# Kernel tuning notes

Hardware: AMD Instinct MI355X
Metric: run time of the kernel (lower is better)

## Reference

```python
import jax, jax.numpy as jnp
import numpy as np

N_NODES = 100000


def setup_inputs() -> dict:
    key = jax.random.key(0)
    ks = jax.random.split(key, 6)
    F_IN, F_CH, F_OUT = 64, 64, 64
    E = 1200000
    x = jax.random.normal(ks[0], (N_NODES, F_IN), dtype=jnp.float32)
    edge_index = jax.random.randint(ks[1], (2, E), 0, N_NODES, dtype=jnp.int64)
    # MLP params (PyTorch Linear default init scale ~ 1/sqrt(fan_in))
    s1 = 1.0 / np.sqrt(2 * F_IN)
    s2 = 1.0 / np.sqrt(F_CH)
    W1 = jax.random.uniform(ks[2], (2 * F_IN, F_CH), jnp.float32, -s1, s1)
    b1 = jax.random.uniform(ks[3], (F_CH,), jnp.float32, -s1, s1)
    W2 = jax.random.uniform(ks[4], (F_CH, F_OUT), jnp.float32, -s2, s2)
    b2 = jax.random.uniform(ks[5], (F_OUT,), jnp.float32, -s2, s2)
    return {"x": x, "edge_index": edge_index, "W1": W1, "b1": b1, "W2": W2, "b2": b2}


def reference(x, edge_index, W1, b1, W2, b2):
    # PyG EdgeConv with aggr='add': out_i = sum_j MLP(concat[x_i, x_j - x_i])
    src = edge_index[0]  # j (source / neighbor)
    dst = edge_index[1]  # i (target, aggregation index)
    x_i = x[dst]                     # [E, F]
    x_j = x[src]                     # [E, F]
    msg = jnp.concatenate([x_i, x_j - x_i], axis=-1)      # [E, 2F]
    h = jax.nn.relu(msg @ W1 + b1) @ W2 + b2               # [E, F_out]
    agg = jax.ops.segment_sum(h, dst, num_segments=N_NODES)  # [N, F_out]
    return jnp.tanh(agg)
```

## Files before the change

kernel.cpp:

```cpp
#include <hip/hip_runtime.h>
#include <math.h>


#define FDIM 64
#define BN 64
#define BSH 6
#define CAPB 1024
#define MAXB 2048
#define EPB 4096
#define PRE_SMEM 24576

typedef unsigned int u32;
typedef unsigned short u16;
typedef _Float16 hf;
typedef _Float16 h2 __attribute__((ext_vector_type(2)));

__device__ __forceinline__ u32 f2h(float f) {
    union { u16 s; hf h; } c; c.h = (hf)f; return (u32)c.s;
}
__device__ __forceinline__ h2 u2h2(u32 u) {
    union { u32 u; h2 h; } c; c.u = u; return c.h;
}

__global__ __launch_bounds__(256) void prep_k(
    const float* __restrict__ x, const float* __restrict__ W1,
    const float* __restrict__ b1, u16* __restrict__ Ah,
    u16* __restrict__ Bmh, const int* __restrict__ ei,
    u32* __restrict__ slotB, int* __restrict__ gcnt,
    int N, int E, int NB, int nPre, int nBin)
{
    __shared__ __align__(16) char smem[PRE_SMEM];
    const int idx = blockIdx.x;
    const int tid = threadIdx.x;

    if ((idx % 6) == 5) {
        const int bb = idx / 6;
        if (bb >= nBin) return;
        int* histL = (int*)smem;
        int* gbase = histL + MAXB;
        const int e0 = bb * EPB;

        for (int j = tid; j < NB; j += 256) histL[j] = 0;
        __syncthreads();

        #pragma unroll 8
        for (int i = 0; i < EPB / 256; ++i) {
            int e = e0 + i * 256 + tid;
            if (e < E) {
                int d = ei[E + e];
                atomicAdd(&histL[d >> BSH], 1);
            }
        }
        __syncthreads();

        for (int j = tid; j < NB; j += 256) {
            int h = histL[j];
            gbase[j] = (h > 0) ? atomicAdd(&gcnt[j], h) : 0;
            histL[j] = 0;
        }
        __syncthreads();

        #pragma unroll 8
        for (int i = 0; i < EPB / 256; ++i) {
            int e = e0 + i * 256 + tid;
            if (e < E) {
                int s = ei[e];
                int d = ei[E + e];
                int b = d >> BSH;
                int pos = gbase[b] + atomicAdd(&histL[b], 1);
                if (pos < CAPB)
                    slotB[(size_t)b * CAPB + pos] =
                        ((u32)(d & (BN - 1)) << 20) | (u32)s;
            }
        }
        return;
    }

    const int pb = idx - idx / 6;
    if (pb >= nPre) return;
    u32 (*Wch)[128] = (u32(*)[128])smem;
    u32* xs = (u32*)(smem + 16384);

    const int node0 = pb * 64;

    for (int i = tid; i < 4096; i += 256) {
        int kk = i >> 7, c = i & 127;
        int k0 = 2 * kk, k1 = k0 + 1;
        float a0, a1;
        if (c < 64) {
            a0 = W1[k0 * 64 + c] - W1[(64 + k0) * 64 + c];
            a1 = W1[k1 * 64 + c] - W1[(64 + k1) * 64 + c];
        } else {
            int cc = c - 64;
            a0 = W1[(64 + k0) * 64 + cc];
            a1 = W1[(64 + k1) * 64 + cc];
        }
        Wch[kk][c] = f2h(a0) | (f2h(a1) << 16);
    }
    {
        const float4* X4 = (const float4*)x;
        #pragma unroll
        for (int it = 0; it < 4; ++it) {
            int i = it * 256 + tid;
            int n = i >> 4, k4 = i & 15;
            int gn = node0 + n;
            float4 v = make_float4(0.f, 0.f, 0.f, 0.f);
            if (gn < N) v = X4[(size_t)gn * 16 + k4];
            int r0 = 2 * k4, r1 = r0 + 1;
            int g = n >> 2, lo = n & 3;
            xs[r0 * 64 + (((g ^ (r0 & 15)) << 2) | lo)] = f2h(v.x) | (f2h(v.y) << 16);
            xs[r1 * 64 + (((g ^ (r1 & 15)) << 2) | lo)] = f2h(v.z) | (f2h(v.w) << 16);
        }
    }
    __syncthreads();

    const int ng = tid & 15, cg = tid >> 4;
    const int n0 = ng * 4, c0 = cg * 8;

    float acc[4][8];
    #pragma unroll
    for (int ci = 0; ci < 8; ++ci) {
        float init = (c0 < 64) ? b1[c0 + ci] : 0.f;
        #pragma unroll
        for (int ni = 0; ni < 4; ++ni) acc[ni][ci] = init;
    }

    #pragma unroll 4
    for (int kk = 0; kk < 32; ++kk) {
        uint4 xq = *(const uint4*)&xs[kk * 64 + ((ng ^ (kk & 15)) << 2)];
        uint4 w0 = *(const uint4*)&Wch[kk][c0];
        uint4 w1 = *(const uint4*)&Wch[kk][c0 + 4];
        h2 wv[8] = {u2h2(w0.x), u2h2(w0.y), u2h2(w0.z), u2h2(w0.w),
                    u2h2(w1.x), u2h2(w1.y), u2h2(w1.z), u2h2(w1.w)};
        u32 xq4[4] = {xq.x, xq.y, xq.z, xq.w};
        #pragma unroll
        for (int ni = 0; ni < 4; ++ni) {
            h2 xh = u2h2(xq4[ni]);
            #pragma unroll
            for (int ci = 0; ci < 8; ++ci)
                acc[ni][ci] = __builtin_amdgcn_fdot2(xh, wv[ci], acc[ni][ci], false);
        }
    }

    #pragma unroll
    for (int ni = 0; ni < 4; ++ni) {
        int n = node0 + n0 + ni;
        if (n >= N) break;
        uint4 pk;
        pk.x = f2h(acc[ni][0]) | (f2h(acc[ni][1]) << 16);
        pk.y = f2h(acc[ni][2]) | (f2h(acc[ni][3]) << 16);
        pk.z = f2h(acc[ni][4]) | (f2h(acc[ni][5]) << 16);
        pk.w = f2h(acc[ni][6]) | (f2h(acc[ni][7]) << 16);
        if (c0 < 64) *(uint4*)&Ah[(size_t)n * 64 + c0] = pk;
        else         *(uint4*)&Bmh[(size_t)n * 64 + (c0 - 64)] = pk;
    }
}

__global__ __launch_bounds__(256) void fused_agg(
    const u16* __restrict__ Ah, const u16* __restrict__ Bmh,
    const u32* __restrict__ slotB, const int* __restrict__ gcnt,
    const float* __restrict__ W2, const float* __restrict__ b2,
    float* __restrict__ out, int N)
{
    __shared__ __align__(16) char uni[16896];
    __shared__ int histL[BN];
    __shared__ int rowO[BN + 1];
    __shared__ int ofs[BN];
    __shared__ float b2s[64];

    uint2* aggTb = (uint2*)uni;
    u32* csrS = (u32*)(uni + 8704);
    u32* eStage = (u32*)(uni + 12800);
    u32* W2kp = (u32*)(uni + 8704);

    const int tid = threadIdx.x;
    const int b = blockIdx.x;
    const int node0 = b * BN;
    const int cntB = min(gcnt[b], CAPB);

    if (tid < 64) b2s[tid] = b2[tid];
    if (tid < BN) histL[tid] = 0;
    __syncthreads();

    for (int i = tid; i < cntB; i += 256) {
        u32 e = slotB[(size_t)b * CAPB + i];
        eStage[i] = e;
        atomicAdd(&histL[e >> 20], 1);
    }
    __syncthreads();

    if (tid < 32) {
        int l = tid;
        int h0 = histL[2 * l], h1 = histL[2 * l + 1];
        int s = h0 + h1, inc = s;
        #pragma unroll
        for (int off = 1; off < 32; off <<= 1) {
            int t = __shfl_up(inc, off);
            if (l >= off) inc += t;
        }
        int base = inc - s;
        rowO[2 * l] = base; rowO[2 * l + 1] = base + h0;
        ofs[2 * l] = base;  ofs[2 * l + 1] = base + h0;
        if (l == 31) rowO[BN] = inc;
    }
    __syncthreads();

    for (int i = tid; i < cntB; i += 256) {
        u32 e = eStage[i];
        int pos = atomicAdd(&ofs[e >> 20], 1);
        csrS[pos] = e & 0xFFFFFu;
    }
    __syncthreads();

    const int q = tid & 15, ng = tid >> 4;
    {
        const uint2* __restrict__ B2 = (const uint2*)Bmh;
        const uint2* __restrict__ A2 = (const uint2*)Ah;
        const h2 SEL10 = {(_Float16)1.f, (_Float16)0.f};
        const h2 SEL01 = {(_Float16)0.f, (_Float16)1.f};
        const h2 HZ = {(_Float16)0.f, (_Float16)0.f};
        #pragma unroll
        for (int h = 0; h < 4; ++h) {
            int nl = ng * 4 + h;
            int gn = node0 + nl;
            int start = rowO[nl];
            int d = (gn < N) ? (rowO[nl + 1] - start) : 0;
            uint2 ua = make_uint2(0u, 0u);
            if (gn < N) ua = A2[(size_t)gn * 16 + q];
            h2 A0 = u2h2(ua.x), A1 = u2h2(ua.y);
            float ac0 = 0.f, ac1 = 0.f, ac2 = 0.f, ac3 = 0.f;

            int j = 0;
            for (; j + 8 <= d; j += 8) {
                int ss[8];
                uint2 bb[8];
                #pragma unroll
                for (int t = 0; t < 8; ++t) ss[t] = csrS[start + j + t];
                #pragma unroll
                for (int t = 0; t < 8; ++t) bb[t] = B2[(size_t)ss[t] * 16 + q];
                #pragma unroll
                for (int t = 0; t < 8; ++t) {
                    h2 t0 = A0 + u2h2(bb[t].x);
                    h2 t1 = A1 + u2h2(bb[t].y);
                    t0 = __builtin_elementwise_max(t0, HZ);
                    t1 = __builtin_elementwise_max(t1, HZ);
                    ac0 = __builtin_amdgcn_fdot2(t0, SEL10, ac0, false);
                    ac1 = __builtin_amdgcn_fdot2(t0, SEL01, ac1, false);
                    ac2 = __builtin_amdgcn_fdot2(t1, SEL10, ac2, false);
                    ac3 = __builtin_amdgcn_fdot2(t1, SEL01, ac3, false);
                }
            }
            if (j < d) {
                int ss[8];
                uint2 bb[8];
                #pragma unroll
                for (int t = 0; t < 8; ++t) ss[t] = csrS[start + min(j + t, d - 1)];
                #pragma unroll
                for (int t = 0; t < 8; ++t) bb[t] = B2[(size_t)ss[t] * 16 + q];
                #pragma unroll
                for (int t = 0; t < 8; ++t) {
                    if (j + t >= d) { bb[t].x = 0xFC00FC00u; bb[t].y = 0xFC00FC00u; }
                    h2 t0 = A0 + u2h2(bb[t].x);
                    h2 t1 = A1 + u2h2(bb[t].y);
                    t0 = __builtin_elementwise_max(t0, HZ);
                    t1 = __builtin_elementwise_max(t1, HZ);
                    ac0 = __builtin_amdgcn_fdot2(t0, SEL10, ac0, false);
                    ac1 = __builtin_amdgcn_fdot2(t0, SEL01, ac1, false);
                    ac2 = __builtin_amdgcn_fdot2(t1, SEL10, ac2, false);
                    ac3 = __builtin_amdgcn_fdot2(t1, SEL01, ac3, false);
                }
            }
            uint2 pk;
            pk.x = f2h(ac0) | (f2h(ac1) << 16);
            pk.y = f2h(ac2) | (f2h(ac3) << 16);
            aggTb[nl * 17 + q] = pk;
        }
    }
    __syncthreads();

    for (int i = tid; i < 2048; i += 256) {
        int kk = i >> 6, c = i & 63;
        W2kp[i] = f2h(W2[(2 * kk) * 64 + c]) | (f2h(W2[(2 * kk + 1) * 64 + c]) << 16);
    }
    __syncthreads();

    {
        const int cg = tid & 15, g = tid >> 4;
        const int c0 = cg * 4;
        const int nb0 = g * 4;
        float o[4][4];
        #pragma unroll
        for (int ni = 0; ni < 4; ++ni) {
            float dg = (float)(rowO[nb0 + ni + 1] - rowO[nb0 + ni]);
            #pragma unroll
            for (int ci = 0; ci < 4; ++ci) o[ni][ci] = dg * b2s[c0 + ci];
        }
        #pragma unroll 4
        for (int kc = 0; kc < 16; ++kc) {
            uint2 u0 = aggTb[(nb0 + 0) * 17 + kc];
            uint2 u1 = aggTb[(nb0 + 1) * 17 + kc];
            uint2 u2 = aggTb[(nb0 + 2) * 17 + kc];
            uint2 u3 = aggTb[(nb0 + 3) * 17 + kc];
            uint4 wA = *(const uint4*)&W2kp[(2 * kc) * 64 + c0];
            uint4 wB = *(const uint4*)&W2kp[(2 * kc + 1) * 64 + c0];
            h2 wa[4] = {u2h2(wA.x), u2h2(wA.y), u2h2(wA.z), u2h2(wA.w)};
            h2 wb[4] = {u2h2(wB.x), u2h2(wB.y), u2h2(wB.z), u2h2(wB.w)};
            h2 a0x = u2h2(u0.x), a0y = u2h2(u0.y);
            h2 a1x = u2h2(u1.x), a1y = u2h2(u1.y);
            h2 a2x = u2h2(u2.x), a2y = u2h2(u2.y);
            h2 a3x = u2h2(u3.x), a3y = u2h2(u3.y);
            #pragma unroll
            for (int ci = 0; ci < 4; ++ci) {
                o[0][ci] = __builtin_amdgcn_fdot2(a0x, wa[ci], o[0][ci], false);
                o[0][ci] = __builtin_amdgcn_fdot2(a0y, wb[ci], o[0][ci], false);
                o[1][ci] = __builtin_amdgcn_fdot2(a1x, wa[ci], o[1][ci], false);
                o[1][ci] = __builtin_amdgcn_fdot2(a1y, wb[ci], o[1][ci], false);
                o[2][ci] = __builtin_amdgcn_fdot2(a2x, wa[ci], o[2][ci], false);
                o[2][ci] = __builtin_amdgcn_fdot2(a2y, wb[ci], o[2][ci], false);
                o[3][ci] = __builtin_amdgcn_fdot2(a3x, wa[ci], o[3][ci], false);
                o[3][ci] = __builtin_amdgcn_fdot2(a3y, wb[ci], o[3][ci], false);
            }
        }
        #pragma unroll
        for (int ni = 0; ni < 4; ++ni) {
            int gn = node0 + nb0 + ni;
            if (gn < N) {
                float4 r = make_float4(tanhf(o[ni][0]), tanhf(o[ni][1]),
                                       tanhf(o[ni][2]), tanhf(o[ni][3]));
                ((float4*)out)[(size_t)gn * 16 + cg] = r;
            }
        }
    }
}

extern "C" void kernel_launch(void* const* d_in, const int* in_sizes, int n_in,
                              void* d_out, int out_size, void* d_ws, size_t ws_size,
                              hipStream_t stream)
{
    const float* x  = (const float*)d_in[0];
    const int*   ei = (const int*)d_in[1];
    const float* W1 = (const float*)d_in[2];
    const float* b1 = (const float*)d_in[3];
    const float* W2 = (const float*)d_in[4];
    const float* b2 = (const float*)d_in[5];
    float* out = (float*)d_out;

    const int N = in_sizes[0] / FDIM;
    const int E = in_sizes[1] / 2;
    const int NB = (N + BN - 1) / BN;

    u16*   Ah    = (u16*)d_ws;
    u16*   Bmh   = Ah + (size_t)N * FDIM;
    u32*   slotB = (u32*)(Bmh + (size_t)N * FDIM);
    int*   gcnt  = (int*)(slotB + (size_t)NB * CAPB);

    hipMemsetAsync(gcnt, 0, (size_t)NB * sizeof(int), stream);

    const int nPre = (N + 63) / 64;
    const int nBin = (E + EPB - 1) / EPB;
    int T = (nPre * 6 + 4) / 5;
    while (T - T / 6 < nPre) ++T;
    if (T < 6 * nBin) T = 6 * nBin;

    prep_k<<<T, 256, 0, stream>>>(x, W1, b1, Ah, Bmh, ei, slotB, gcnt,
                                  N, E, NB, nPre, nBin);
    fused_agg<<<NB, 256, 0, stream>>>(Ah, Bmh, slotB, gcnt, W2, b2, out, N);
}
```

Before: 166.2 us.

## Merge memset, prep and aggregation into one cooperative persistent kernel

Replaces the memset plus two kernel launches with a single cooperative kernel that uses grid-wide syncs between zeroing the counters, the binning and node-projection phase, and the aggregation phase. Blocks loop persistently over work items, sized by occupancy times CU count. The aim is to remove launch overhead and inter-kernel gaps. In exchange, every block waits at each grid barrier, the grid is capped by occupancy, and the larger merged shared-memory pool may lower occupancy in the aggregation phase. The original launch path is kept as a fallback if the cooperative launch fails.

```diff
diff --git a/kernel.cpp b/kernel.cpp
--- a/kernel.cpp
+++ b/kernel.cpp
@@ -1,5 +1,8 @@
 #include <hip/hip_runtime.h>
+#include <hip/hip_cooperative_groups.h>
 #include <math.h>
+
+namespace cg = cooperative_groups;
 
 
 #define FDIM 64
@@ -8,7 +11,7 @@
 #define CAPB 1024
 #define MAXB 2048
 #define EPB 4096
-#define PRE_SMEM 24576
+#define POOLB 24576
 
 typedef unsigned int u32;
 typedef unsigned short u16;
@@ -22,62 +25,56 @@
     union { u32 u; h2 h; } c; c.u = u; return c.h;
 }
 
-__global__ __launch_bounds__(256) void prep_k(
+
+__device__ __forceinline__ void bin_body(
+    char* smem, int tid, int bb, const int* __restrict__ ei,
+    u32* __restrict__ slotB, int* __restrict__ gcnt, int E, int NB)
+{
+    int* histL = (int*)smem;
+    int* gbase = histL + MAXB;
+    const int e0 = bb * EPB;
+
+    for (int j = tid; j < NB; j += 256) histL[j] = 0;
+    __syncthreads();
+
+    #pragma unroll 8
+    for (int i = 0; i < EPB / 256; ++i) {
+        int e = e0 + i * 256 + tid;
+        if (e < E) {
+            int d = ei[E + e];
+            atomicAdd(&histL[d >> BSH], 1);
+        }
+    }
+    __syncthreads();
+
+    for (int j = tid; j < NB; j += 256) {
+        int h = histL[j];
+        gbase[j] = (h > 0) ? atomicAdd(&gcnt[j], h) : 0;
+        histL[j] = 0;
+    }
+    __syncthreads();
+
+    #pragma unroll 8
+    for (int i = 0; i < EPB / 256; ++i) {
+        int e = e0 + i * 256 + tid;
+        if (e < E) {
+            int s = ei[e];
+            int d = ei[E + e];
+            int b = d >> BSH;
+            int pos = gbase[b] + atomicAdd(&histL[b], 1);
+            if (pos < CAPB)
+                slotB[(size_t)b * CAPB + pos] =
+                    ((u32)(d & (BN - 1)) << 20) | (u32)s;
+        }
+    }
+}
+
+__device__ __forceinline__ void node_body(
+    char* smem, int tid, int pb,
     const float* __restrict__ x, const float* __restrict__ W1,
     const float* __restrict__ b1, u16* __restrict__ Ah,
-    u16* __restrict__ Bmh, const int* __restrict__ ei,
-    u32* __restrict__ slotB, int* __restrict__ gcnt,
-    int N, int E, int NB, int nPre, int nBin)
-{
-    __shared__ __align__(16) char smem[PRE_SMEM];
-    const int idx = blockIdx.x;
-    const int tid = threadIdx.x;
-
-    if ((idx % 6) == 5) {
-        const int bb = idx / 6;
-        if (bb >= nBin) return;
-        int* histL = (int*)smem;
-        int* gbase = histL + MAXB;
-        const int e0 = bb * EPB;
-
-        for (int j = tid; j < NB; j += 256) histL[j] = 0;
-        __syncthreads();
-
-        #pragma unroll 8
-        for (int i = 0; i < EPB / 256; ++i) {
-            int e = e0 + i * 256 + tid;
-            if (e < E) {
-                int d = ei[E + e];
-                atomicAdd(&histL[d >> BSH], 1);
-            }
-        }
-        __syncthreads();
-
-        for (int j = tid; j < NB; j += 256) {
-            int h = histL[j];
-            gbase[j] = (h > 0) ? atomicAdd(&gcnt[j], h) : 0;
-            histL[j] = 0;
-        }
-        __syncthreads();
-
-        #pragma unroll 8
-        for (int i = 0; i < EPB / 256; ++i) {
-            int e = e0 + i * 256 + tid;
-            if (e < E) {
-                int s = ei[e];
-                int d = ei[E + e];
-                int b = d >> BSH;
-                int pos = gbase[b] + atomicAdd(&histL[b], 1);
-                if (pos < CAPB)
-                    slotB[(size_t)b * CAPB + pos] =
-                        ((u32)(d & (BN - 1)) << 20) | (u32)s;
-            }
-        }
-        return;
-    }
-
-    const int pb = idx - idx / 6;
-    if (pb >= nPre) return;
+    u16* __restrict__ Bmh, int N)
+{
     u32 (*Wch)[128] = (u32(*)[128])smem;
     u32* xs = (u32*)(smem + 16384);
 
@@ -156,27 +153,20 @@
     }
 }
 
-__global__ __launch_bounds__(256) void fused_agg(
+__device__ __forceinline__ void agg_body(
+    char* uni, int* histL, int* rowO, int* ofs, float* b2s,
+    int tid, int b, int cntB,
     const u16* __restrict__ Ah, const u16* __restrict__ Bmh,
-    const u32* __restrict__ slotB, const int* __restrict__ gcnt,
+    const u32* __restrict__ slotB,
     const float* __restrict__ W2, const float* __restrict__ b2,
     float* __restrict__ out, int N)
 {
-    __shared__ __align__(16) char uni[16896];
-    __shared__ int histL[BN];
-    __shared__ int rowO[BN + 1];
-    __shared__ int ofs[BN];
-    __shared__ float b2s[64];
-
     uint2* aggTb = (uint2*)uni;
     u32* csrS = (u32*)(uni + 8704);
     u32* eStage = (u32*)(uni + 12800);
     u32* W2kp = (u32*)(uni + 8704);
 
-    const int tid = threadIdx.x;
-    const int b = blockIdx.x;
     const int node0 = b * BN;
-    const int cntB = min(gcnt[b], CAPB);
 
     if (tid < 64) b2s[tid] = b2[tid];
     if (tid < BN) histL[tid] = 0;
@@ -285,8 +275,8 @@
     __syncthreads();
 
     {
-        const int cg = tid & 15, g = tid >> 4;
-        const int c0 = cg * 4;
+        const int cg2 = tid & 15, g = tid >> 4;
+        const int c0 = cg2 * 4;
         const int nb0 = g * 4;
         float o[4][4];
         #pragma unroll
@@ -327,10 +317,91 @@
             if (gn < N) {
                 float4 r = make_float4(tanhf(o[ni][0]), tanhf(o[ni][1]),
                                        tanhf(o[ni][2]), tanhf(o[ni][3]));
-                ((float4*)out)[(size_t)gn * 16 + cg] = r;
+                ((float4*)out)[(size_t)gn * 16 + cg2] = r;
             }
         }
     }
+}
+
+__global__ __launch_bounds__(256) void fused_all(
+    const float* __restrict__ x, const float* __restrict__ W1,
+    const float* __restrict__ b1, const float* __restrict__ W2,
+    const float* __restrict__ b2, const int* __restrict__ ei,
+    u16* __restrict__ Ah, u16* __restrict__ Bmh,
+    u32* __restrict__ slotB, int* __restrict__ gcnt,
+    float* __restrict__ out,
+    int N, int E, int NB, int nPre, int nBin, int T)
+{
+    cg::grid_group gg = cg::this_grid();
+    __shared__ __align__(16) char pool[POOLB];
+    __shared__ int histL[BN];
+    __shared__ int rowO[BN + 1];
+    __shared__ int ofs[BN];
+    __shared__ float b2s[64];
+    const int tid = threadIdx.x;
+
+    for (int i = blockIdx.x * 256 + tid; i < NB; i += gridDim.x * 256)
+        gcnt[i] = 0;
+    gg.sync();
+
+    for (int v = blockIdx.x; v < T; v += gridDim.x) {
+        __syncthreads();
+        if ((v % 6) == 5) {
+            int bb = v / 6;
+            if (bb < nBin) bin_body(pool, tid, bb, ei, slotB, gcnt, E, NB);
+        } else {
+            int pb = v - v / 6;
+            if (pb < nPre) node_body(pool, tid, pb, x, W1, b1, Ah, Bmh, N);
+        }
+    }
+    __threadfence();
+    gg.sync();
+
+    for (int b = blockIdx.x; b < NB; b += gridDim.x) {
+        __syncthreads();
+        int cntB = min(atomicAdd(&gcnt[b], 0), CAPB);
+        agg_body(pool, histL, rowO, ofs, b2s, tid, b, cntB,
+                 Ah, Bmh, slotB, W2, b2, out, N);
+    }
+}
+
+__global__ __launch_bounds__(256) void prep_k(
+    const float* __restrict__ x, const float* __restrict__ W1,
+    const float* __restrict__ b1, u16* __restrict__ Ah,
+    u16* __restrict__ Bmh, const int* __restrict__ ei,
+    u32* __restrict__ slotB, int* __restrict__ gcnt,
+    int N, int E, int NB, int nPre, int nBin)
+{
+    __shared__ __align__(16) char smem[POOLB];
+    const int idx = blockIdx.x;
+    const int tid = threadIdx.x;
+    if ((idx % 6) == 5) {
+        const int bb = idx / 6;
+        if (bb >= nBin) return;
+        bin_body(smem, tid, bb, ei, slotB, gcnt, E, NB);
+        return;
+    }
+    const int pb = idx - idx / 6;
+    if (pb >= nPre) return;
+    node_body(smem, tid, pb, x, W1, b1, Ah, Bmh, N);
+}
+
+__global__ __launch_bounds__(256) void fused_agg(
+    const u16* __restrict__ Ah, const u16* __restrict__ Bmh,
+    const u32* __restrict__ slotB, const int* __restrict__ gcnt,
+    const float* __restrict__ W2, const float* __restrict__ b2,
+    float* __restrict__ out, int N)
+{
+    __shared__ __align__(16) char uni[16896];
+    __shared__ int histL[BN];
+    __shared__ int rowO[BN + 1];
+    __shared__ int ofs[BN];
+    __shared__ float b2s[64];
+    const int tid = threadIdx.x;
+    const int b = blockIdx.x;
+    int cntB = min(gcnt[b], CAPB);
+    agg_body(uni, histL, rowO, ofs, b2s, tid, b, cntB,
+             Ah, Bmh, slotB, W2, b2, out, N);
 }
 
 extern "C" void kernel_launch(void* const* d_in, const int* in_sizes, int n_in,
@@ -354,15 +425,40 @@
     u32*   slotB = (u32*)(Bmh + (size_t)N * FDIM);
     int*   gcnt  = (int*)(slotB + (size_t)NB * CAPB);
 
-    hipMemsetAsync(gcnt, 0, (size_t)NB * sizeof(int), stream);
-
     const int nPre = (N + 63) / 64;
     const int nBin = (E + EPB - 1) / EPB;
     int T = (nPre * 6 + 4) / 5;
     while (T - T / 6 < nPre) ++T;
     if (T < 6 * nBin) T = 6 * nBin;
 
-    prep_k<<<T, 256, 0, stream>>>(x, W1, b1, Ah, Bmh, ei, slotB, gcnt,
-                                  N, E, NB, nPre, nBin);
-    fused_agg<<<NB, 256, 0, stream>>>(Ah, Bmh, slotB, gcnt, W2, b2, out, N);
-}
+    static int coopGrid = 0;
+    if (coopGrid == 0) {
+        int perCU = 0;
+        hipError_t e1 = hipOccupancyMaxActiveBlocksPerMultiprocessor(
+            &perCU, fused_all, 256, 0);
+        int dev = 0;
+        hipGetDevice(&dev);
+        int nCU = 0;
+        hipError_t e2 = hipDeviceGetAttribute(
+            &nCU, hipDeviceAttributeMultiprocessorCount, dev);
+        if (e1 != hipSuccess || perCU <= 0) perCU = 4;
+        if (e2 != hipSuccess || nCU <= 0) nCU = 256;
+        coopGrid = perCU * nCU;
+    }
+
+    void* args[] = {
+        (void*)&x, (void*)&W1, (void*)&b1, (void*)&W2, (void*)&b2,
+        (void*)&ei, (void*)&Ah, (void*)&Bmh, (void*)&slotB, (void*)&gcnt,
+        (void*)&out, (void*)&N, (void*)&E, (void*)&NB,
+        (void*)&nPre, (void*)&nBin, (void*)&T
+    };
+    hipError_t err = hipLaunchCooperativeKernel(
+        (void*)fused_all, dim3(coopGrid), dim3(256), args, 0, stream);
+
+    if (err != hipSuccess) {
+        hipMemsetAsync(gcnt, 0, (size_t)NB * sizeof(int), stream);
+        prep_k<<<T, 256, 0, stream>>>(x, W1, b1, Ah, Bmh, ei, slotB, gcnt,
+                                      N, E, NB, nPre, nBin);
+        fused_agg<<<NB, 256, 0, stream>>>(Ah, Bmh, slotB, gcnt, W2, b2, out, N);
+    }
+}
```

After: 366.2 us. 2.2x slower.
